# Performance work log

Measured on AMD Instinct MI355X. Metric: run time of the kernel, lower is better.

Reference implementation:

```python
import jax, jax.numpy as jnp
import numpy as np

NC = 80
REG_MAX = 16
NO = REG_MAX * 4 + NC  # 144
LEVEL_SHAPES = [(80, 80), (40, 40), (20, 20)]
STRIDES = [8.0, 16.0, 32.0]
CHANNELS = [256, 512, 512]


def _make_anchors():
    """Returns anchor_points (2, A) and stride_tensor (1, A), grid offset 0.5."""
    pts, sts = [], []
    for (h, w), s in zip(LEVEL_SHAPES, STRIDES):
        sx = jnp.arange(w, dtype=jnp.float32) + 0.5
        sy = jnp.arange(h, dtype=jnp.float32) + 0.5
        gy, gx = jnp.meshgrid(sy, sx, indexing='ij')
        pts.append(jnp.stack([gx.ravel(), gy.ravel()], axis=-1))  # (h*w, 2)
        sts.append(jnp.full((h * w,), s, dtype=jnp.float32))
    anchors = jnp.concatenate(pts, axis=0).T          # (2, A)
    strides = jnp.concatenate(sts, axis=0)[None, :]   # (1, A)
    return anchors, strides


def setup_inputs() -> dict:
    key = jax.random.key(0)
    ks = jax.random.split(key, 16)
    inp = {}
    inp['x0'] = jax.random.normal(ks[0], (16, 256, 80, 80), dtype=jnp.float32)
    inp['x1'] = jax.random.normal(ks[1], (16, 512, 40, 40), dtype=jnp.float32)
    inp['x2'] = jax.random.normal(ks[2], (16, 512, 20, 20), dtype=jnp.float32)
    # per-level 1x1 conv head weights: box branch (4*reg_max out), cls branch (nc out)
    for i, c in enumerate(CHANNELS):
        sc = 1.0 / np.sqrt(c)
        inp[f'w_box{i}'] = jax.random.normal(ks[3 + 4 * i], (REG_MAX * 4, c), dtype=jnp.float32) * sc
        inp[f'b_box{i}'] = jax.random.normal(ks[4 + 4 * i], (REG_MAX * 4,), dtype=jnp.float32) * 0.01
        inp[f'w_cls{i}'] = jax.random.normal(ks[5 + 4 * i], (NC, c), dtype=jnp.float32) * sc
        inp[f'b_cls{i}'] = jax.random.normal(ks[6 + 4 * i], (NC,), dtype=jnp.float32) * 0.01
    return inp


def _level_out(x, wb, bb, wc, bc):
    # cat(cv2(x), cv3(x), dim=1) then view(B, no, -1)
    box = jnp.einsum('bchw,oc->bohw', x, wb) + bb[None, :, None, None]
    cls = jnp.einsum('bchw,oc->bohw', x, wc) + bc[None, :, None, None]
    B = x.shape[0]
    return jnp.concatenate([box, cls], axis=1).reshape(B, NO, -1)


def reference(x0, x1, x2,
              w_box0, b_box0, w_cls0, b_cls0,
              w_box1, b_box1, w_cls1, b_cls1,
              w_box2, b_box2, w_cls2, b_cls2):
    xs = [x0, x1, x2]
    wbs = [w_box0, w_box1, w_box2]
    bbs = [b_box0, b_box1, b_box2]
    wcs = [w_cls0, w_cls1, w_cls2]
    bcs = [b_cls0, b_cls1, b_cls2]
    x_cat = jnp.concatenate(
        [_level_out(x, wb, bb, wc, bc) for x, wb, bb, wc, bc in zip(xs, wbs, bbs, wcs, bcs)],
        axis=2)  # (B, 144, A)
    B, _, A = x_cat.shape
    box, cls = x_cat[:, :REG_MAX * 4, :], x_cat[:, REG_MAX * 4:, :]

    # DFL: (B, 4*16, A) -> softmax over 16 bins -> expected distance per side
    p = jax.nn.softmax(box.reshape(B, 4, REG_MAX, A), axis=2)
    dist = jnp.einsum('bkra,r->bka', p, jnp.arange(REG_MAX, dtype=jnp.float32))  # (B, 4, A)

    # dist2bbox (xywh) on anchor grid, scale by stride
    anchors, strides = _make_anchors()
    anc = anchors[None]                 # (1, 2, A)
    lt, rb = dist[:, :2, :], dist[:, 2:, :]
    x1y1 = anc - lt
    x2y2 = anc + rb
    c_xy = (x1y1 + x2y2) * 0.5
    wh = x2y2 - x1y1
    dbox = jnp.concatenate([c_xy, wh], axis=1) * strides[:, None, :]  # (B, 4, A)

    # boxes (B, A, 4), scores (B, A, nc) -- the tensors fed to EfficientNMS_TRT
    boxes = jnp.transpose(dbox, (0, 2, 1))
    scores = jnp.transpose(cls, (0, 2, 1))
    return jnp.concatenate([boxes, scores], axis=-1)  # (B, A, 4 + nc)
```

## Files before the change

kernel.cpp:

```cpp
#include <hip/hip_runtime.h>


typedef __bf16 bf16x8 __attribute__((ext_vector_type(8)));
typedef float  f32x4  __attribute__((ext_vector_type(4)));

#define NTHREADS 256

#define WCHUNK 9216
#define WOFF0 0
#define WOFF1 73728
#define WOFF2 221184

#define XBUF 16384

__device__ __forceinline__ unsigned int pack_bf16(float a, float b) {
    unsigned int ua = __builtin_bit_cast(unsigned int, a);
    unsigned int ub = __builtin_bit_cast(unsigned int, b);
    return ((ua + 0x8000u) >> 16) | ((ub + 0x8000u) & 0xffff0000u);
}

__device__ __forceinline__ void gload_lds16(const void* g, void* l) {
    __builtin_amdgcn_global_load_lds(
        (const __attribute__((address_space(1))) void*)g,
        (__attribute__((address_space(3))) void*)l, 16, 0, 0);
}

__global__ __launch_bounds__(256)
void prep_w_kernel(const float* __restrict__ wb0, const float* __restrict__ wc0,
                   const float* __restrict__ wb1, const float* __restrict__ wc1,
                   const float* __restrict__ wb2, const float* __restrict__ wc2,
                   unsigned char* __restrict__ ws) {
    int uid = blockIdx.x * 256 + threadIdx.x;
    if (uid >= 23040) return;
    const float* wb; const float* wc; int C; size_t off; int uu;
    if (uid < 4608)       { wb = wb0; wc = wc0; C = 256; off = WOFF0; uu = uid; }
    else if (uid < 13824) { wb = wb1; wc = wc1; C = 512; off = WOFF1; uu = uid - 4608; }
    else                  { wb = wb2; wc = wc2; C = 512; off = WOFF2; uu = uid - 13824; }
    const int kunits = C / 8;
    const int row = uu / kunits;
    const int k   = (uu % kunits) * 8;
    const float* src = ((row < 64) ? (wb + row * C) : (wc + (row - 64) * C)) + k;
    const float4 f0 = *(const float4*)(src);
    const float4 f1 = *(const float4*)(src + 4);
    uint4 p;
    p.x = pack_bf16(f0.x, f0.y);
    p.y = pack_bf16(f0.z, f0.w);
    p.z = pack_bf16(f1.x, f1.y);
    p.w = pack_bf16(f1.z, f1.w);
    const int kc   = k >> 5;
    const int m    = row >> 4;
    const int lane = (row & 15) | (((k & 31) >> 3) << 4);
    *(uint4*)(ws + off + (size_t)kc * WCHUNK + m * 1024 + lane * 16) = p;
}

__global__ __launch_bounds__(NTHREADS, 3)
void UltralyticsDetect_kernel(
        const float* __restrict__ x0, const float* __restrict__ x1, const float* __restrict__ x2,
        const unsigned char* __restrict__ wimg,
        const float* __restrict__ bb0, const float* __restrict__ bc0,
        const float* __restrict__ bb1, const float* __restrict__ bc1,
        const float* __restrict__ bb2, const float* __restrict__ bc2,
        float* __restrict__ out) {

    __shared__ __align__(16) unsigned char s_x[2 * XBUF];

    const int bid = blockIdx.x;
    const float* x; const float* bbox; const float* bcls;
    int C, GW, HW, AOFF, TPB, rb; float STRIDE; size_t WOFF;
    if (bid < 208) {
        x = x1; bbox = bb1; bcls = bc1; rb = bid;
        C = 512; GW = 40; HW = 1600; AOFF = 6400; TPB = 13; STRIDE = 16.0f; WOFF = WOFF1;
    } else if (bid < 272) {
        x = x2; bbox = bb2; bcls = bc2; rb = bid - 208;
        C = 512; GW = 20; HW = 400;  AOFF = 8000; TPB = 4;  STRIDE = 32.0f; WOFF = WOFF2;
    } else {
        x = x0; bbox = bb0; bcls = bc0; rb = bid - 272;
        C = 256; GW = 80; HW = 6400; AOFF = 0;    TPB = 50; STRIDE = 8.0f;  WOFF = WOFF0;
    }
    const int nkc = C / 32;

    const int b    = rb / TPB;
    const int tile = rb - b * TPB;
    int hw0 = tile * 128;
    if (hw0 > HW - 128) hw0 = HW - 128;

    const int tid  = threadIdx.x;
    const int wv   = tid >> 6;
    const int lane = tid & 63;
    const int col  = lane & 15;
    const int q4   = lane >> 4;

    const float* xlev = x + (size_t)b * C * HW;
    const unsigned char* wlev = wimg + WOFF + (size_t)lane * 16;

    const int xg  = (((lane & 31) ^ (wv << 2)) << 2);
    const int xr  = lane >> 5;
    const int xrd0 = (((wv * 32 + col) << 2) ^ (q4 << 6)) + q4 * 8 * 512;
    const int xrd1 = (((wv * 32 + 16 + col) << 2) ^ (q4 << 6)) + q4 * 8 * 512;

    f32x4 acc[9][2];
#pragma unroll
    for (int m = 0; m < 9; ++m) {
        acc[m][0] = (f32x4){0.f, 0.f, 0.f, 0.f};
        acc[m][1] = (f32x4){0.f, 0.f, 0.f, 0.f};
    }

#define XDMA(CC, BUF)                                                       \
    {                                                                       \
        _Pragma("unroll")                                                   \
        for (int _i = 0; _i < 4; ++_i) {                                    \
            const int _r2 = wv * 8 + _i * 2;                                \
            gload_lds16(xlev + (size_t)((CC) * 32 + _r2 + xr) * HW + hw0 + xg, \
                        s_x + (BUF) * XBUF + _r2 * 512);                    \
        }                                                                   \
    }

    XDMA(0, 0);
    __syncthreads();

    for (int kc = 0; kc < nkc; ++kc) {
        if (kc + 1 < nkc) XDMA(kc + 1, (kc & 1) ^ 1);

        const unsigned char* xbuf = s_x + (kc & 1) * XBUF;
        float xf0[8], xf1[8];
#pragma unroll
        for (int j = 0; j < 8; ++j) {
            xf0[j] = *(const float*)(xbuf + xrd0 + j * 512);
            xf1[j] = *(const float*)(xbuf + xrd1 + j * 512);
        }
        uint4 qa, qb;
        qa.x = pack_bf16(xf0[0], xf0[1]); qa.y = pack_bf16(xf0[2], xf0[3]);
        qa.z = pack_bf16(xf0[4], xf0[5]); qa.w = pack_bf16(xf0[6], xf0[7]);
        qb.x = pack_bf16(xf1[0], xf1[1]); qb.y = pack_bf16(xf1[2], xf1[3]);
        qb.z = pack_bf16(xf1[4], xf1[5]); qb.w = pack_bf16(xf1[6], xf1[7]);
        const bf16x8 fA = __builtin_bit_cast(bf16x8, qa);
        const bf16x8 fB = __builtin_bit_cast(bf16x8, qb);

        const unsigned char* wk = wlev + (size_t)kc * WCHUNK;
#pragma unroll
        for (int m = 0; m < 9; ++m) {
            const bf16x8 a_ = *(const bf16x8*)(wk + m * 1024);
            acc[m][0] = __builtin_amdgcn_mfma_f32_16x16x32_bf16(a_, fA, acc[m][0], 0, 0, 0);
            acc[m][1] = __builtin_amdgcn_mfma_f32_16x16x32_bf16(a_, fB, acc[m][1], 0, 0, 0);
        }

        __syncthreads();
    }

#undef XDMA

    float4 bcv[5];
#pragma unroll
    for (int m = 0; m < 5; ++m)
        bcv[m] = *(const float4*)(bcls + m * 16 + q4 * 4);

    const float LOG2E = 1.44269504088896f;

#pragma unroll
    for (int nf = 0; nf < 2; ++nf) {
        const int alocal = wv * 32 + nf * 16 + col;
        const int hw = hw0 + alocal;

        float dist[4];
#pragma unroll
        for (int g = 0; g < 4; ++g) {
            const float4 bbv = *(const float4*)(bbox + g * 16 + q4 * 4);
            const float v0 = acc[g][nf][0] + bbv.x;
            const float v1 = acc[g][nf][1] + bbv.y;
            const float v2 = acc[g][nf][2] + bbv.z;
            const float v3 = acc[g][nf][3] + bbv.w;
            float mx = fmaxf(fmaxf(v0, v1), fmaxf(v2, v3));
            mx = fmaxf(mx, __shfl_xor(mx, 16));
            mx = fmaxf(mx, __shfl_xor(mx, 32));
            const float e0 = __builtin_amdgcn_exp2f((v0 - mx) * LOG2E);
            const float e1 = __builtin_amdgcn_exp2f((v1 - mx) * LOG2E);
            const float e2 = __builtin_amdgcn_exp2f((v2 - mx) * LOG2E);
            const float e3 = __builtin_amdgcn_exp2f((v3 - mx) * LOG2E);
            float s  = e0 + e1 + e2 + e3;
            float ws = e1 + 2.f * e2 + 3.f * e3 + (float)(q4 * 4) * s;
            s  += __shfl_xor(s, 16);
            s  += __shfl_xor(s, 32);
            ws += __shfl_xor(ws, 16);
            ws += __shfl_xor(ws, 32);
            dist[g] = ws / s;
        }

        const size_t obase = ((size_t)b * 8400 + AOFF + hw) * 84;
        if (q4 == 0) {
            const float ax = (float)(hw % GW) + 0.5f;
            const float ay = (float)(hw / GW) + 0.5f;
            f32x4 bx;
            bx[0] = (ax + 0.5f * (dist[2] - dist[0])) * STRIDE;
            bx[1] = (ay + 0.5f * (dist[3] - dist[1])) * STRIDE;
            bx[2] = (dist[0] + dist[2]) * STRIDE;
            bx[3] = (dist[1] + dist[3]) * STRIDE;
            *(f32x4*)(out + obase) = bx;
        }
#pragma unroll
        for (int m = 0; m < 5; ++m) {
            f32x4 v;
            v[0] = acc[m + 4][nf][0] + bcv[m].x;
            v[1] = acc[m + 4][nf][1] + bcv[m].y;
            v[2] = acc[m + 4][nf][2] + bcv[m].z;
            v[3] = acc[m + 4][nf][3] + bcv[m].w;
            *(f32x4*)(out + obase + 4 + m * 16 + q4 * 4) = v;
        }
    }
}

extern "C" void kernel_launch(void* const* d_in, const int* in_sizes, int n_in,
                              void* d_out, int out_size, void* d_ws, size_t ws_size,
                              hipStream_t stream) {
    const float* x0  = (const float*)d_in[0];
    const float* x1  = (const float*)d_in[1];
    const float* x2  = (const float*)d_in[2];
    const float* wb0 = (const float*)d_in[3];
    const float* bb0 = (const float*)d_in[4];
    const float* wc0 = (const float*)d_in[5];
    const float* bc0 = (const float*)d_in[6];
    const float* wb1 = (const float*)d_in[7];
    const float* bb1 = (const float*)d_in[8];
    const float* wc1 = (const float*)d_in[9];
    const float* bc1 = (const float*)d_in[10];
    const float* wb2 = (const float*)d_in[11];
    const float* bb2 = (const float*)d_in[12];
    const float* wc2 = (const float*)d_in[13];
    const float* bc2 = (const float*)d_in[14];

    unsigned char* wimg = (unsigned char*)d_ws;

    prep_w_kernel<<<90, 256, 0, stream>>>(wb0, wc0, wb1, wc1, wb2, wc2, wimg);

    UltralyticsDetect_kernel<<<1072, NTHREADS, 0, stream>>>(
        x0, x1, x2, wimg,
        bb0, bc0, bb1, bc1, bb2, bc2,
        (float*)d_out);
}
```

Measured before the change: 59.60 us.

## Replace LDS double-buffering with register-prefetched direct global loads

Removes the shared-memory staging of activations and its per-chunk barriers. Each lane now loads its activation values straight from global memory into registers. The K loop is unrolled by two with ping-pong register sets, so the activation and weight loads for the next chunk are issued before the current MFMAs run. This drops the LDS round-trip and block syncs, but raises register pressure and relies on scalar 4-byte strided global loads, which coalesce across lanes but may be less efficient than the 16-byte DMA path.

```diff
diff --git a/kernel.cpp b/kernel.cpp
--- a/kernel.cpp
+++ b/kernel.cpp
@@ -11,18 +11,10 @@
 #define WOFF1 73728
 #define WOFF2 221184
 
-#define XBUF 16384
-
 __device__ __forceinline__ unsigned int pack_bf16(float a, float b) {
     unsigned int ua = __builtin_bit_cast(unsigned int, a);
     unsigned int ub = __builtin_bit_cast(unsigned int, b);
     return ((ua + 0x8000u) >> 16) | ((ub + 0x8000u) & 0xffff0000u);
-}
-
-__device__ __forceinline__ void gload_lds16(const void* g, void* l) {
-    __builtin_amdgcn_global_load_lds(
-        (const __attribute__((address_space(1))) void*)g,
-        (__attribute__((address_space(3))) void*)l, 16, 0, 0);
 }
 
 __global__ __launch_bounds__(256)
@@ -62,8 +54,6 @@
         const float* __restrict__ bb2, const float* __restrict__ bc2,
         float* __restrict__ out) {
 
-    __shared__ __align__(16) unsigned char s_x[2 * XBUF];
-
     const int bid = blockIdx.x;
     const float* x; const float* bbox; const float* bcls;
     int C, GW, HW, AOFF, TPB, rb; float STRIDE; size_t WOFF;
@@ -90,13 +80,11 @@
     const int col  = lane & 15;
     const int q4   = lane >> 4;
 
-    const float* xlev = x + (size_t)b * C * HW;
+    const char* xbyte = (const char*)(x + (size_t)b * C * HW + hw0);
+    const int a0 = wv * 32 + col;
+    const int voff0 = (a0 + q4 * 8 * HW) * 4;
+    const int voff1 = voff0 + 16 * 4;
     const unsigned char* wlev = wimg + WOFF + (size_t)lane * 16;
-
-    const int xg  = (((lane & 31) ^ (wv << 2)) << 2);
-    const int xr  = lane >> 5;
-    const int xrd0 = (((wv * 32 + col) << 2) ^ (q4 << 6)) + q4 * 8 * 512;
-    const int xrd1 = (((wv * 32 + 16 + col) << 2) ^ (q4 << 6)) + q4 * 8 * 512;
 
     f32x4 acc[9][2];
 #pragma unroll
@@ -105,49 +93,71 @@
         acc[m][1] = (f32x4){0.f, 0.f, 0.f, 0.f};
     }
 
-#define XDMA(CC, BUF)                                                       \
-    {                                                                       \
+    float P0[8], P1[8], Q0[8], Q1[8];
+    bf16x8 WE[9], WO[9];
+
+#define XLOAD(V0, V1, CC)                                                   \
+    {                                                                       \
+        const char* _xb = xbyte + (size_t)(CC) * 32 * HW * 4;               \
         _Pragma("unroll")                                                   \
-        for (int _i = 0; _i < 4; ++_i) {                                    \
-            const int _r2 = wv * 8 + _i * 2;                                \
-            gload_lds16(xlev + (size_t)((CC) * 32 + _r2 + xr) * HW + hw0 + xg, \
-                        s_x + (BUF) * XBUF + _r2 * 512);                    \
+        for (int _j = 0; _j < 8; ++_j) {                                    \
+            V0[_j] = *(const float*)(_xb + voff0 + _j * HW * 4);            \
+            V1[_j] = *(const float*)(_xb + voff1 + _j * HW * 4);            \
         }                                                                   \
     }
 
-    XDMA(0, 0);
-    __syncthreads();
-
-    for (int kc = 0; kc < nkc; ++kc) {
-        if (kc + 1 < nkc) XDMA(kc + 1, (kc & 1) ^ 1);
-
-        const unsigned char* xbuf = s_x + (kc & 1) * XBUF;
-        float xf0[8], xf1[8];
-#pragma unroll
-        for (int j = 0; j < 8; ++j) {
-            xf0[j] = *(const float*)(xbuf + xrd0 + j * 512);
-            xf1[j] = *(const float*)(xbuf + xrd1 + j * 512);
-        }
-        uint4 qa, qb;
-        qa.x = pack_bf16(xf0[0], xf0[1]); qa.y = pack_bf16(xf0[2], xf0[3]);
-        qa.z = pack_bf16(xf0[4], xf0[5]); qa.w = pack_bf16(xf0[6], xf0[7]);
-        qb.x = pack_bf16(xf1[0], xf1[1]); qb.y = pack_bf16(xf1[2], xf1[3]);
-        qb.z = pack_bf16(xf1[4], xf1[5]); qb.w = pack_bf16(xf1[6], xf1[7]);
-        const bf16x8 fA = __builtin_bit_cast(bf16x8, qa);
-        const bf16x8 fB = __builtin_bit_cast(bf16x8, qb);
-
-        const unsigned char* wk = wlev + (size_t)kc * WCHUNK;
-#pragma unroll
-        for (int m = 0; m < 9; ++m) {
-            const bf16x8 a_ = *(const bf16x8*)(wk + m * 1024);
-            acc[m][0] = __builtin_amdgcn_mfma_f32_16x16x32_bf16(a_, fA, acc[m][0], 0, 0, 0);
-            acc[m][1] = __builtin_amdgcn_mfma_f32_16x16x32_bf16(a_, fB, acc[m][1], 0, 0, 0);
-        }
-
-        __syncthreads();
-    }
-
-#undef XDMA
+#define WLOAD(WF, CC)                                                       \
+    {                                                                       \
+        const unsigned char* _wk = wlev + (size_t)(CC) * WCHUNK;            \
+        _Pragma("unroll")                                                   \
+        for (int _m = 0; _m < 9; ++_m)                                      \
+            WF[_m] = *(const bf16x8*)(_wk + _m * 1024);                     \
+    }
+
+#define CVT(V, DST)                                                         \
+    {                                                                       \
+        uint4 _q;                                                           \
+        _q.x = pack_bf16(V[0], V[1]);                                       \
+        _q.y = pack_bf16(V[2], V[3]);                                       \
+        _q.z = pack_bf16(V[4], V[5]);                                       \
+        _q.w = pack_bf16(V[6], V[7]);                                       \
+        DST = __builtin_bit_cast(bf16x8, _q);                               \
+    }
+
+#define MFMA18(WF, FA, FB)                                                  \
+    {                                                                       \
+        _Pragma("unroll")                                                   \
+        for (int _m = 0; _m < 9; ++_m) {                                    \
+            acc[_m][0] = __builtin_amdgcn_mfma_f32_16x16x32_bf16(WF[_m], FA, acc[_m][0], 0, 0, 0); \
+            acc[_m][1] = __builtin_amdgcn_mfma_f32_16x16x32_bf16(WF[_m], FB, acc[_m][1], 0, 0, 0); \
+        }                                                                   \
+    }
+
+    XLOAD(P0, P1, 0);
+    WLOAD(WE, 0);
+
+    for (int kc2 = 0; kc2 < nkc; kc2 += 2) {
+        bf16x8 fA, fB;
+
+        XLOAD(Q0, Q1, kc2 + 1);
+        WLOAD(WO, kc2 + 1);
+        CVT(P0, fA);
+        CVT(P1, fB);
+        MFMA18(WE, fA, fB);
+
+        if (kc2 + 2 < nkc) {
+            XLOAD(P0, P1, kc2 + 2);
+            WLOAD(WE, kc2 + 2);
+        }
+        CVT(Q0, fA);
+        CVT(Q1, fB);
+        MFMA18(WO, fA, fB);
+    }
+
+#undef MFMA18
+#undef CVT
+#undef WLOAD
+#undef XLOAD
 
     float4 bcv[5];
 #pragma unroll
```

Result: slower. 130.0 us (+118.2%).

## Stage bf16 X and weights in swizzled LDS with 512-thread 256-anchor tiles

Applied to the files above, without the earlier changes.

Doubles the anchor tile per block to 256 with 8 waves. Activations are now loaded into registers, converted to bf16 once, and written to swizzled LDS, replacing the raw fp32 DMA that every wave re-read and re-converted. Weight chunks are also DMA'd into double-buffered swizzled LDS instead of being read straight from global memory per MFMA. This aims to cut redundant conversion work and global weight traffic, at the cost of more LDS, register pressure, and a grid half the size.

```diff
diff --git a/kernel.cpp b/kernel.cpp
--- a/kernel.cpp
+++ b/kernel.cpp
@@ -4,7 +4,7 @@
 typedef __bf16 bf16x8 __attribute__((ext_vector_type(8)));
 typedef float  f32x4  __attribute__((ext_vector_type(4)));
 
-#define NTHREADS 256
+#define NTHREADS 512
 
 #define WCHUNK 9216
 #define WOFF0 0
@@ -17,6 +17,10 @@
     unsigned int ua = __builtin_bit_cast(unsigned int, a);
     unsigned int ub = __builtin_bit_cast(unsigned int, b);
     return ((ua + 0x8000u) >> 16) | ((ub + 0x8000u) & 0xffff0000u);
+}
+
+__device__ __forceinline__ int swz32(int row, int kbyte) {
+    return row * 64 + (kbyte ^ ((((row & 3) ^ ((row >> 2) & 1))) << 4));
 }
 
 __device__ __forceinline__ void gload_lds16(const void* g, void* l) {
@@ -47,13 +51,12 @@
     p.y = pack_bf16(f0.z, f0.w);
     p.z = pack_bf16(f1.x, f1.y);
     p.w = pack_bf16(f1.z, f1.w);
-    const int kc   = k >> 5;
-    const int m    = row >> 4;
-    const int lane = (row & 15) | (((k & 31) >> 3) << 4);
-    *(uint4*)(ws + off + (size_t)kc * WCHUNK + m * 1024 + lane * 16) = p;
-}
-
-__global__ __launch_bounds__(NTHREADS, 3)
+    const int chunk = k >> 5;
+    const int kg    = (k & 31) >> 3;
+    *(uint4*)(ws + off + (size_t)chunk * WCHUNK + swz32(row, kg * 16)) = p;
+}
+
+__global__ __launch_bounds__(NTHREADS, 4)
 void UltralyticsDetect_kernel(
         const float* __restrict__ x0, const float* __restrict__ x1, const float* __restrict__ x2,
         const unsigned char* __restrict__ wimg,
@@ -62,27 +65,28 @@
         const float* __restrict__ bb2, const float* __restrict__ bc2,
         float* __restrict__ out) {
 
+    __shared__ __align__(16) unsigned char s_w[2 * WCHUNK];
     __shared__ __align__(16) unsigned char s_x[2 * XBUF];
 
     const int bid = blockIdx.x;
     const float* x; const float* bbox; const float* bcls;
     int C, GW, HW, AOFF, TPB, rb; float STRIDE; size_t WOFF;
-    if (bid < 208) {
+    if (bid < 112) {
         x = x1; bbox = bb1; bcls = bc1; rb = bid;
-        C = 512; GW = 40; HW = 1600; AOFF = 6400; TPB = 13; STRIDE = 16.0f; WOFF = WOFF1;
-    } else if (bid < 272) {
-        x = x2; bbox = bb2; bcls = bc2; rb = bid - 208;
-        C = 512; GW = 20; HW = 400;  AOFF = 8000; TPB = 4;  STRIDE = 32.0f; WOFF = WOFF2;
+        C = 512; GW = 40; HW = 1600; AOFF = 6400; TPB = 7;  STRIDE = 16.0f; WOFF = WOFF1;
+    } else if (bid < 144) {
+        x = x2; bbox = bb2; bcls = bc2; rb = bid - 112;
+        C = 512; GW = 20; HW = 400;  AOFF = 8000; TPB = 2;  STRIDE = 32.0f; WOFF = WOFF2;
     } else {
-        x = x0; bbox = bb0; bcls = bc0; rb = bid - 272;
-        C = 256; GW = 80; HW = 6400; AOFF = 0;    TPB = 50; STRIDE = 8.0f;  WOFF = WOFF0;
+        x = x0; bbox = bb0; bcls = bc0; rb = bid - 144;
+        C = 256; GW = 80; HW = 6400; AOFF = 0;    TPB = 25; STRIDE = 8.0f;  WOFF = WOFF0;
     }
     const int nkc = C / 32;
 
     const int b    = rb / TPB;
     const int tile = rb - b * TPB;
-    int hw0 = tile * 128;
-    if (hw0 > HW - 128) hw0 = HW - 128;
+    int hw0 = tile * 256;
+    if (hw0 > HW - 256) hw0 = HW - 256;
 
     const int tid  = threadIdx.x;
     const int wv   = tid >> 6;
@@ -91,12 +95,19 @@
     const int q4   = lane >> 4;
 
     const float* xlev = x + (size_t)b * C * HW;
-    const unsigned char* wlev = wimg + WOFF + (size_t)lane * 16;
-
-    const int xg  = (((lane & 31) ^ (wv << 2)) << 2);
-    const int xr  = lane >> 5;
-    const int xrd0 = (((wv * 32 + col) << 2) ^ (q4 << 6)) + q4 * 8 * 512;
-    const int xrd1 = (((wv * 32 + 16 + col) << 2) ^ (q4 << 6)) + q4 * 8 * 512;
+    const unsigned char* wlev = wimg + WOFF;
+
+    const int sa = (wv & 3) * 64 + lane;
+    const int sg = wv >> 2;
+    const float* xsrc = xlev + hw0 + sa;
+    const int swzb  = (((sa & 3) ^ ((sa >> 2) & 1))) << 4;
+    const int xw0   = sa * 64 + ((sg * 32) ^ swzb);
+    const int xw1   = sa * 64 + ((sg * 32 + 16) ^ swzb);
+
+    const int a0 = wv * 32 + col;
+    const int a1 = a0 + 16;
+    const int xr0 = swz32(a0, q4 * 16);
+    const int xr1 = swz32(a1, q4 * 16);
 
     f32x4 acc[9][2];
 #pragma unroll
@@ -105,41 +116,58 @@
         acc[m][1] = (f32x4){0.f, 0.f, 0.f, 0.f};
     }
 
-#define XDMA(CC, BUF)                                                       \
+    float S[16];
+
+#define XLOADS(CC)                                                          \
     {                                                                       \
+        const float* _p = xsrc + (size_t)((CC) * 32 + sg * 16) * HW;        \
         _Pragma("unroll")                                                   \
-        for (int _i = 0; _i < 4; ++_i) {                                    \
-            const int _r2 = wv * 8 + _i * 2;                                \
-            gload_lds16(xlev + (size_t)((CC) * 32 + _r2 + xr) * HW + hw0 + xg, \
-                        s_x + (BUF) * XBUF + _r2 * 512);                    \
-        }                                                                   \
-    }
-
-    XDMA(0, 0);
+        for (int _m = 0; _m < 16; ++_m)                                     \
+            S[_m] = _p[(size_t)_m * HW];                                    \
+    }
+
+#define XWRITE(BUF)                                                         \
+    {                                                                       \
+        uint4 _w0, _w1;                                                     \
+        _w0.x = pack_bf16(S[0],  S[1]);  _w0.y = pack_bf16(S[2],  S[3]);    \
+        _w0.z = pack_bf16(S[4],  S[5]);  _w0.w = pack_bf16(S[6],  S[7]);    \
+        _w1.x = pack_bf16(S[8],  S[9]);  _w1.y = pack_bf16(S[10], S[11]);   \
+        _w1.z = pack_bf16(S[12], S[13]); _w1.w = pack_bf16(S[14], S[15]);   \
+        *(uint4*)(s_x + (BUF) * XBUF + xw0) = _w0;                          \
+        *(uint4*)(s_x + (BUF) * XBUF + xw1) = _w1;                          \
+    }
+
+#define WDMA(CC, BUF)                                                       \
+    {                                                                       \
+        gload_lds16(wlev + (size_t)(CC) * WCHUNK + tid * 16,                \
+                    s_w + (BUF) * WCHUNK + tid * 16);                       \
+        if (tid < 64)                                                       \
+            gload_lds16(wlev + (size_t)(CC) * WCHUNK + (512 + tid) * 16,    \
+                        s_w + (BUF) * WCHUNK + (512 + tid) * 16);           \
+    }
+
+    XLOADS(0);
+    XWRITE(0);
+    WDMA(0, 0);
+    XLOADS(1);
     __syncthreads();
 
     for (int kc = 0; kc < nkc; ++kc) {
-        if (kc + 1 < nkc) XDMA(kc + 1, (kc & 1) ^ 1);
-
-        const unsigned char* xbuf = s_x + (kc & 1) * XBUF;
-        float xf0[8], xf1[8];
-#pragma unroll
-        for (int j = 0; j < 8; ++j) {
-            xf0[j] = *(const float*)(xbuf + xrd0 + j * 512);
-            xf1[j] = *(const float*)(xbuf + xrd1 + j * 512);
-        }
-        uint4 qa, qb;
-        qa.x = pack_bf16(xf0[0], xf0[1]); qa.y = pack_bf16(xf0[2], xf0[3]);
-        qa.z = pack_bf16(xf0[4], xf0[5]); qa.w = pack_bf16(xf0[6], xf0[7]);
-        qb.x = pack_bf16(xf1[0], xf1[1]); qb.y = pack_bf16(xf1[2], xf1[3]);
-        qb.z = pack_bf16(xf1[4], xf1[5]); qb.w = pack_bf16(xf1[6], xf1[7]);
-        const bf16x8 fA = __builtin_bit_cast(bf16x8, qa);
-        const bf16x8 fB = __builtin_bit_cast(bf16x8, qb);
-
-        const unsigned char* wk = wlev + (size_t)kc * WCHUNK;
+        const int buf = kc & 1;
+
+        if (kc + 1 < nkc) {
+            XWRITE(buf ^ 1);
+            WDMA(kc + 1, buf ^ 1);
+        }
+        if (kc + 2 < nkc) XLOADS(kc + 2);
+
+        const bf16x8 fA = *(const bf16x8*)(s_x + buf * XBUF + xr0);
+        const bf16x8 fB = *(const bf16x8*)(s_x + buf * XBUF + xr1);
+
+        const unsigned char* wbuf = s_w + buf * WCHUNK;
 #pragma unroll
         for (int m = 0; m < 9; ++m) {
-            const bf16x8 a_ = *(const bf16x8*)(wk + m * 1024);
+            const bf16x8 a_ = *(const bf16x8*)(wbuf + swz32(m * 16 + col, q4 * 16));
             acc[m][0] = __builtin_amdgcn_mfma_f32_16x16x32_bf16(a_, fA, acc[m][0], 0, 0, 0);
             acc[m][1] = __builtin_amdgcn_mfma_f32_16x16x32_bf16(a_, fB, acc[m][1], 0, 0, 0);
         }
@@ -147,7 +175,9 @@
         __syncthreads();
     }
 
-#undef XDMA
+#undef WDMA
+#undef XWRITE
+#undef XLOADS
 
     float4 bcv[5];
 #pragma unroll
@@ -231,7 +261,7 @@
 
     prep_w_kernel<<<90, 256, 0, stream>>>(wb0, wc0, wb1, wc1, wb2, wc2, wimg);
 
-    UltralyticsDetect_kernel<<<1072, NTHREADS, 0, stream>>>(
+    UltralyticsDetect_kernel<<<544, NTHREADS, 0, stream>>>(
         x0, x1, x2, wimg,
         bb0, bc0, bb1, bc1, bb2, bc2,
         (float*)d_out);
```

Result: faster. 54.48 us (-8.6%).
